# Kernel optimization log

Hardware: AMD Instinct MI355X
Metric: run time of the kernel (lower is better)

## Reference

```python
import jax, jax.numpy as jnp
import numpy as np

B, S, D, H = 4, 2048, 2048, 16
DH = D // H  # 128
BASE = 10000.0


def _rope_tables(seq_len, d_head, dtype):
    # inv_freq over even indices of half-dim, freqs duplicated (cat(freqs, freqs))
    inv_freq = 1.0 / (BASE ** (jnp.arange(0, d_head, 2, dtype=jnp.float32) / d_head))
    t = jnp.arange(seq_len, dtype=jnp.float32)
    freqs = jnp.einsum('i,j->ij', t, inv_freq)          # [S, d_head/2]
    emb = jnp.concatenate([freqs, freqs], axis=-1)       # [S, d_head]
    return jnp.cos(emb).astype(dtype), jnp.sin(emb).astype(dtype)


def _rotate_half(x):
    x1, x2 = jnp.split(x, 2, axis=-1)
    return jnp.concatenate([-x2, x1], axis=-1)


def setup_inputs() -> dict:
    key = jax.random.key(0)
    k1, k2, k3 = jax.random.split(key, 3)
    x = jax.random.normal(k1, (B, S, D), dtype=jnp.float32)
    Wqkv = jax.random.normal(k2, (3 * D, D), dtype=jnp.float32) * (D ** -0.5)
    Wo = jax.random.normal(k3, (D, D), dtype=jnp.float32) * (D ** -0.5)
    return {"x": x, "Wqkv": Wqkv, "Wo": Wo}


def reference(x, Wqkv, Wo) -> jnp.ndarray:
    b, s, d = x.shape
    # fused QKV projection: Linear(d, 3d, bias=False) -> x @ Wqkv.T
    qkv = jnp.einsum('bsd,ed->bse', x, Wqkv)                      # [B,S,3D]
    qkv = qkv.reshape(b, s, 3, H, DH)                              # (n n_head d_head)
    q = jnp.transpose(qkv[:, :, 0], (0, 2, 1, 3))                  # [B,H,S,DH]
    k = jnp.transpose(qkv[:, :, 1], (0, 2, 1, 3))
    v = jnp.transpose(qkv[:, :, 2], (0, 2, 1, 3))
    # rotary position embedding
    cos, sin = _rope_tables(s, DH, x.dtype)                        # [S,DH]
    cos = cos[None, None, :, :]
    sin = sin[None, None, :, :]
    q = q * cos + _rotate_half(q) * sin
    k = k * cos + _rotate_half(k) * sin
    # eval-path manual causal attention
    scale = 1.0 / jnp.sqrt(jnp.asarray(DH, dtype=x.dtype))
    scores = jnp.einsum('bhqd,bhkd->bhqk', q, k) * scale           # [B,H,S,S]
    causal = jnp.tril(jnp.ones((s, s), dtype=bool))
    scores = jnp.where(causal[None, None, :, :], scores, -jnp.inf)
    pattern = jax.nn.softmax(scores, axis=-1)
    z = jnp.einsum('bhqk,bhkd->bhqd', pattern, v)                  # [B,H,S,DH]
    z = jnp.transpose(z, (0, 2, 1, 3)).reshape(b, s, d)            # [B,S,D]
    return jnp.einsum('bsd,ed->bse', z, Wo)
```

## Files before the change

### kernel.cpp

```cpp
#include <hip/hip_runtime.h>
#include <hip/hip_bf16.h>
#include <stdint.h>

#define B_ 4
#define S_ 2048
#define D_ 2048
#define H_ 16
#define DH_ 128

typedef short bf8_t __attribute__((ext_vector_type(8)));
typedef float f4_t  __attribute__((ext_vector_type(4)));

__device__ __forceinline__ unsigned short f2bf(float f) {
  __hip_bfloat16 h = __float2bfloat16(f);
  return *reinterpret_cast<const unsigned short*>(&h);
}
__device__ __forceinline__ float bf2f(unsigned short u) {
  return __uint_as_float(((unsigned int)u) << 16);
}

__device__ __forceinline__ void gload_lds16(const void* g, void* lds) {
  __builtin_amdgcn_global_load_lds(
      (const __attribute__((address_space(1))) unsigned int*)(uintptr_t)g,
      (__attribute__((address_space(3))) unsigned int*)(unsigned int)(uintptr_t)lds,
      16, 0, 0);
}

__global__ __launch_bounds__(256) void conv_bf16(const float* __restrict__ in,
                                                 unsigned short* __restrict__ out,
                                                 int n4) {
  int i = blockIdx.x * 256 + threadIdx.x;
  if (i >= n4) return;
  float4 v = ((const float4*)in)[i];
  ushort4 u;
  u.x = f2bf(v.x); u.y = f2bf(v.y); u.z = f2bf(v.z); u.w = f2bf(v.w);
  ((ushort4*)out)[i] = u;
}

template <int EPI>
__global__ __launch_bounds__(512, 2) void gemm256(
    const unsigned short* __restrict__ A, const unsigned short* __restrict__ Bt,
    float* __restrict__ Cf, unsigned short* __restrict__ Cb,
    int M, int N, int K) {
  __shared__ unsigned short AB[4][2][8192];
  const int tid  = threadIdx.x;
  const int lane = tid & 63;
  const int wv   = tid >> 6;
  const int wr   = wv >> 2;
  const int wc   = wv & 3;
  const int rsel = lane & 15;
  const int g    = lane >> 4;
  const int qr0  = g * 4;

  int id  = blockIdx.y * gridDim.x + blockIdx.x;
  int cpx = (gridDim.x * gridDim.y) >> 3;
  int swz = (id & 7) * cpx + (id >> 3);
  const int bm = (swz / gridDim.x) * 256;
  const int bn = (swz % gridDim.x) * 256;

  const int NS = K >> 5;

  const int ob0 = tid * 16, ob1 = ob0 + 8192;
  const int row0 = ob0 >> 6, row1 = ob1 >> 6;
  const int g0 = ((ob0 >> 4) & 3) ^ ((row0 >> 1) & 3);
  const int g1 = ((ob1 >> 4) & 3) ^ ((row1 >> 1) & 3);
  const unsigned short* Ag0 = A + (size_t)(bm + row0) * K + g0 * 8;
  const unsigned short* Ag1 = A + (size_t)(bm + row1) * K + g1 * 8;
  const unsigned short* Bg0 = Bt + (size_t)(bn + row0) * K + g0 * 8;
  const unsigned short* Bg1 = Bt + (size_t)(bn + row1) * K + g1 * 8;

  f4_t acc[8][4];
#pragma unroll
  for (int i = 0; i < 8; ++i)
#pragma unroll
    for (int j = 0; j < 4; ++j) acc[i][j] = (f4_t){0.f, 0.f, 0.f, 0.f};

  int aoff[8], boff[4];
#pragma unroll
  for (int i = 0; i < 8; ++i) {
    int arow = wr * 128 + i * 16 + rsel;
    aoff[i] = arow * 64 + ((g * 16) ^ ((arow & 6) << 3));
  }
#pragma unroll
  for (int j = 0; j < 4; ++j) {
    int brow = wc * 64 + j * 16 + rsel;
    boff[j] = brow * 64 + ((g * 16) ^ ((brow & 6) << 3));
  }

#define STAGE(sl)                                                        \
  {                                                                      \
    int slot_ = (sl) & 3;                                                \
    int ks_   = (sl) << 5;                                               \
    gload_lds16(Ag0 + ks_, (char*)&AB[slot_][0][0] + ob0);               \
    gload_lds16(Ag1 + ks_, (char*)&AB[slot_][0][0] + ob1);               \
    gload_lds16(Bg0 + ks_, (char*)&AB[slot_][1][0] + ob0);               \
    gload_lds16(Bg1 + ks_, (char*)&AB[slot_][1][0] + ob1);               \
  }

  STAGE(0); STAGE(1); STAGE(2);

  for (int s = 0; s < NS; ++s) {
    if (s < NS - 2)       asm volatile("s_waitcnt vmcnt(8)" ::: "memory");
    else if (s == NS - 2) asm volatile("s_waitcnt vmcnt(4)" ::: "memory");
    else                  asm volatile("s_waitcnt vmcnt(0)" ::: "memory");
    __builtin_amdgcn_s_barrier();
    asm volatile("" ::: "memory");

    const char* As_ = (const char*)&AB[s & 3][0][0];
    const char* Bs_ = (const char*)&AB[s & 3][1][0];
    bf8_t af[8], bfr[4];
#pragma unroll
    for (int i = 0; i < 8; ++i) af[i] = *(const bf8_t*)(As_ + aoff[i]);
#pragma unroll
    for (int j = 0; j < 4; ++j) bfr[j] = *(const bf8_t*)(Bs_ + boff[j]);

    if (s + 3 < NS) STAGE(s + 3);

    __builtin_amdgcn_s_setprio(1);
#pragma unroll
    for (int i = 0; i < 8; ++i)
#pragma unroll
      for (int j = 0; j < 4; ++j)
        acc[i][j] = __builtin_amdgcn_mfma_f32_16x16x32_bf16(af[i], bfr[j], acc[i][j], 0, 0, 0);
    __builtin_amdgcn_s_setprio(0);
  }
#undef STAGE

#pragma unroll
  for (int i = 0; i < 8; ++i) {
#pragma unroll
    for (int j = 0; j < 4; ++j) {
#pragma unroll
      for (int r = 0; r < 4; ++r) {
        int row = bm + wr * 128 + i * 16 + qr0 + r;
        int col = bn + wc * 64 + j * 16 + rsel;
        float v = acc[i][j][r];
        if (EPI == 0) {
          Cf[(size_t)row * N + col] = v;
        } else {
          int c = col >> 11, h = (col >> 7) & (H_ - 1), dh = col & (DH_ - 1);
          int b = row >> 11, s = row & (S_ - 1);
          size_t dst = ((((size_t)c * B_ + b) * H_ + h) * S_ + s) * DH_ + dh;
          Cb[dst] = f2bf(v);
        }
      }
    }
  }
}

__global__ void rope_tab(float* __restrict__ tc, float* __restrict__ ts) {
  int s = blockIdx.x;
  int i = threadIdx.x;
  float inv = powf(10000.0f, -(float)i / 64.0f);
  float f   = (float)s * inv;
  tc[s * 64 + i] = cosf(f);
  ts[s * 64 + i] = sinf(f);
}

__global__ __launch_bounds__(256) void rope_apply(
    unsigned short* __restrict__ Q, unsigned short* __restrict__ Kk,
    const float* __restrict__ tc, const float* __restrict__ ts) {
  int idx  = blockIdx.x * 256 + threadIdx.x;
  int i    = idx & 63;
  int s    = (idx >> 6) & (S_ - 1);
  int bh   = (idx >> 17) & 63;
  int tsel = idx >> 23;
  unsigned short* T = tsel ? Kk : Q;
  size_t base = ((size_t)bh * S_ + s) * DH_;
  float x1 = bf2f(T[base + i]);
  float x2 = bf2f(T[base + i + 64]);
  float c  = tc[s * 64 + i], sn = ts[s * 64 + i];
  T[base + i]      = f2bf(x1 * c - x2 * sn);
  T[base + i + 64] = f2bf(x2 * c + x1 * sn);
}

__global__ __launch_bounds__(512) void attn_fwd(
    const unsigned short* __restrict__ Q, const unsigned short* __restrict__ Kk,
    const unsigned short* __restrict__ V, unsigned short* __restrict__ Z) {
  __shared__ unsigned short Ks[3][64 * 128];
  __shared__ unsigned short Vt[2][128 * 64];
  __shared__ unsigned short Pw[8][16 * 64];
  const int tid  = threadIdx.x;
  const int lane = tid & 63;
  const int wv   = tid >> 6;

  int id = blockIdx.y * gridDim.x + blockIdx.x;
  int sw = (id & 7) * ((gridDim.x * gridDim.y) >> 3) + (id >> 3);
  const int bh = sw >> 4;
  const int q0 = (15 - (sw & 15)) * 128;

  const size_t base = (size_t)bh * S_ * DH_;
  const int rsel = lane & 15;
  const int g    = lane >> 4;
  const int kof  = g * 8;
  const int qr0  = g * 4;
  const int qlo  = q0 + wv * 16;
  const int qhi  = qlo + 15;
  const int qrow = qlo + rsel;
  const float sl2 = 0.08838834764831845f * 1.4426950408889634f;

  bf8_t aq[4];
#pragma unroll
  for (int kc = 0; kc < 4; ++kc) {
    aq[kc] = *(const bf8_t*)&Q[base + (size_t)qrow * DH_ + kc * 32 + kof];
#pragma unroll
    for (int e = 0; e < 8; ++e)
      aq[kc][e] = (short)f2bf(bf2f((unsigned short)aq[kc][e]) * sl2);
  }

  bf8_t vones;
#pragma unroll
  for (int e = 0; e < 8; ++e) vones[e] = (short)0x3F80;

  f4_t o[9];
#pragma unroll
  for (int nf = 0; nf < 9; ++nf) o[nf] = (f4_t){0.f, 0.f, 0.f, 0.f};
  float mrow[4] = {-3e30f, -3e30f, -3e30f, -3e30f};
  const int nt = q0 / 64 + 2;

  const int kvp = tid & 31;
  const int vc0 = (tid >> 5) * 8;

#define KSTAGE(tt)                                                            \
  {                                                                           \
    const unsigned short* gK_ = Kk + base + (size_t)(tt) * 64 * DH_;          \
    int slot_ = (tt) % 3;                                                     \
    _Pragma("unroll")                                                         \
    for (int c = 0; c < 2; ++c) {                                             \
      int ob = (c * 512 + tid) * 16;                                          \
      int row = ob >> 8;                                                      \
      int scol = (ob & 255) ^ ((row & 7) << 4);                               \
      gload_lds16(gK_ + (size_t)row * DH_ + (scol >> 1),                      \
                  (char*)&Ks[slot_][0] + ob);                                 \
    }                                                                         \
  }
#define VTWRITE(buf_)                                                         \
  {                                                                           \
    unsigned int* Vt32 = (unsigned int*)&Vt[buf_][0];                         \
    _Pragma("unroll")                                                         \
    for (int e = 0; e < 8; ++e) {                                             \
      unsigned int val = (unsigned short)vlo[e] |                             \
                         ((unsigned int)(unsigned short)vhi[e] << 16);        \
      Vt32[(vc0 + e) * 32 + (kvp ^ (e << 2))] = val;                          \
    }                                                                         \
  }

  bf8_t vlo, vhi;
  vlo = *(const bf8_t*)&V[base + (size_t)(2 * kvp) * DH_ + vc0];
  vhi = *(const bf8_t*)&V[base + (size_t)(2 * kvp + 1) * DH_ + vc0];
  KSTAGE(0);
  KSTAGE(1);
  VTWRITE(0);

  for (int t = 0; t < nt; ++t) {
    const int curV = t & 1;
    const int curK = t % 3;
    const bool pfV = (t + 1 < nt);
    const bool pfK = (t + 2 < nt);

    if (pfV) asm volatile("s_waitcnt vmcnt(2)" ::: "memory");
    else     asm volatile("s_waitcnt vmcnt(0)" ::: "memory");
    asm volatile("s_waitcnt lgkmcnt(0)" ::: "memory");
    __builtin_amdgcn_s_barrier();
    asm volatile("" ::: "memory");

    if (pfV) {
      const unsigned short* gV = V + base + (size_t)(t + 1) * 64 * DH_;
      vlo = *(const bf8_t*)&gV[(size_t)(2 * kvp) * DH_ + vc0];
      vhi = *(const bf8_t*)&gV[(size_t)(2 * kvp + 1) * DH_ + vc0];
    }
    if (pfK) KSTAGE(t + 2);

    const int kv0 = t * 64;
    const bool active = (kv0 <= qhi);
    const bool domask = active && (kv0 + 63 > qlo);

    if (active) {
      f4_t sacc[4];
#pragma unroll
      for (int cf = 0; cf < 4; ++cf) sacc[cf] = (f4_t){0.f, 0.f, 0.f, 0.f};
      __builtin_amdgcn_s_setprio(1);
#pragma unroll
      for (int cf = 0; cf < 4; ++cf)
#pragma unroll
        for (int kc = 0; kc < 4; ++kc) {
          int krow = cf * 16 + rsel;
          bf8_t bk = *(const bf8_t*)&Ks[curK][krow * 128 + ((kc * 32 + kof) ^ ((krow & 7) << 3))];
          sacc[cf] = __builtin_amdgcn_mfma_f32_16x16x32_bf16(aq[kc], bk, sacc[cf], 0, 0, 0);
        }
      __builtin_amdgcn_s_setprio(0);

      if (domask) {
#pragma unroll
        for (int cf = 0; cf < 4; ++cf) {
          int kvabs = kv0 + cf * 16 + rsel;
#pragma unroll
          for (int r = 0; r < 4; ++r) {
            int qabs = qlo + qr0 + r;
            if (kvabs > qabs) sacc[cf][r] = -3e30f;
          }
        }
      }

      float tmr[4];
#pragma unroll
      for (int r = 0; r < 4; ++r)
        tmr[r] = fmaxf(fmaxf(sacc[0][r], sacc[1][r]), fmaxf(sacc[2][r], sacc[3][r]));
      bool needr = (tmr[0] > mrow[0] + 11.f) || (tmr[1] > mrow[1] + 11.f) ||
                   (tmr[2] > mrow[2] + 11.f) || (tmr[3] > mrow[3] + 11.f);
      if (__any(needr)) {
#pragma unroll
        for (int r = 0; r < 4; ++r) {
          float m = tmr[r];
#pragma unroll
          for (int d = 1; d < 16; d <<= 1) m = fmaxf(m, __shfl_xor(m, d, 16));
          float nm = fmaxf(mrow[r], m);
          float sc = exp2f(mrow[r] - nm);
          mrow[r] = nm;
#pragma unroll
          for (int nf = 0; nf < 9; ++nf) o[nf][r] *= sc;
        }
      }
#pragma unroll
      for (int cf = 0; cf < 4; ++cf)
#pragma unroll
        for (int r = 0; r < 4; ++r)
          sacc[cf][r] = exp2f(sacc[cf][r] - mrow[r]);

      unsigned short* P = &Pw[wv][0];
#pragma unroll
      for (int cf = 0; cf < 4; ++cf)
#pragma unroll
        for (int r = 0; r < 4; ++r) {
          int prow = qr0 + r;
          P[prow * 64 + ((cf * 16 + rsel) ^ ((prow >> 1) << 3))] = f2bf(sacc[cf][r]);
        }
    }

    if (pfV) VTWRITE(curV ^ 1);

    if (active) {
      unsigned short* P = &Pw[wv][0];
      __builtin_amdgcn_s_setprio(1);
#pragma unroll
      for (int kc2 = 0; kc2 < 2; ++kc2) {
        bf8_t pa = *(const bf8_t*)&P[rsel * 64 + ((kc2 * 32 + kof) ^ ((rsel >> 1) << 3))];
#pragma unroll
        for (int nf = 0; nf < 8; ++nf) {
          int vrow = nf * 16 + rsel;
          bf8_t bv = *(const bf8_t*)&Vt[curV][vrow * 64 + ((kc2 * 32 + kof) ^ ((vrow & 7) << 3))];
          o[nf] = __builtin_amdgcn_mfma_f32_16x16x32_bf16(pa, bv, o[nf], 0, 0, 0);
        }
        o[8] = __builtin_amdgcn_mfma_f32_16x16x32_bf16(pa, vones, o[8], 0, 0, 0);
      }
      __builtin_amdgcn_s_setprio(0);
    }
  }
#undef KSTAGE
#undef VTWRITE

  const int b = bh >> 4, h = bh & 15;
#pragma unroll
  for (int r = 0; r < 4; ++r) {
    float inv = 1.0f / o[8][r];
    int s = qlo + qr0 + r;
    size_t rowo = ((size_t)b * S_ + s) * D_ + h * DH_;
#pragma unroll
    for (int nf = 0; nf < 8; ++nf)
      Z[rowo + nf * 16 + rsel] = f2bf(o[nf][r] * inv);
  }
}

extern "C" void kernel_launch(void* const* d_in, const int* in_sizes, int n_in,
                              void* d_out, int out_size, void* d_ws, size_t ws_size,
                              hipStream_t stream) {
  const float* x    = (const float*)d_in[0];
  const float* Wqkv = (const float*)d_in[1];
  const float* Wo   = (const float*)d_in[2];
  float* out = (float*)d_out;

  const size_t QKV_ELEMS = (size_t)B_ * H_ * S_ * DH_;
  char* w = (char*)d_ws;
  unsigned short* xb = (unsigned short*)w;
  unsigned short* z  = xb;
  w += (size_t)8192 * 2048 * 2;
  unsigned short* wqkvb = (unsigned short*)w; w += (size_t)6144 * 2048 * 2;
  unsigned short* wob   = (unsigned short*)w; w += (size_t)2048 * 2048 * 2;
  unsigned short* qq = (unsigned short*)w;    w += QKV_ELEMS * 2;
  unsigned short* kk = (unsigned short*)w;    w += QKV_ELEMS * 2;
  unsigned short* vv = (unsigned short*)w;    w += QKV_ELEMS * 2;
  float* tabc = (float*)w; w += (size_t)S_ * 64 * 4;
  float* tabs = (float*)w; w += (size_t)S_ * 64 * 4;
  if ((size_t)(w - (char*)d_ws) > ws_size) return;

  conv_bf16<<<16384, 256, 0, stream>>>(x, xb, 8192 * 2048 / 4);
  conv_bf16<<<12288, 256, 0, stream>>>(Wqkv, wqkvb, 6144 * 2048 / 4);
  conv_bf16<<<4096, 256, 0, stream>>>(Wo, wob, 2048 * 2048 / 4);
  gemm256<1><<<dim3(24, 32), 512, 0, stream>>>(xb, wqkvb, nullptr, qq, 8192, 6144, 2048);
  rope_tab<<<2048, 64, 0, stream>>>(tabc, tabs);
  rope_apply<<<65536, 256, 0, stream>>>(qq, kk, tabc, tabs);
  attn_fwd<<<dim3(S_ / 128, B_ * H_), 512, 0, stream>>>(qq, kk, vv, z);
  gemm256<0><<<dim3(8, 32), 512, 0, stream>>>(z, wob, out, nullptr, 8192, 2048, 2048);
}
```

Baseline: 495.7 us.

## Process 32 query rows per wave to double K/V tile reuse in attention

Result: faster. 431.1 us (-13.0%).

```diff
diff --git a/kernel.cpp b/kernel.cpp
--- a/kernel.cpp
+++ b/kernel.cpp
@@ -179,44 +179,51 @@
     const unsigned short* __restrict__ V, unsigned short* __restrict__ Z) {
   __shared__ unsigned short Ks[3][64 * 128];
   __shared__ unsigned short Vt[2][128 * 64];
-  __shared__ unsigned short Pw[8][16 * 64];
+  __shared__ unsigned short Pw[8][32 * 64];
   const int tid  = threadIdx.x;
   const int lane = tid & 63;
   const int wv   = tid >> 6;
 
-  int id = blockIdx.y * gridDim.x + blockIdx.x;
-  int sw = (id & 7) * ((gridDim.x * gridDim.y) >> 3) + (id >> 3);
-  const int bh = sw >> 4;
-  const int q0 = (15 - (sw & 15)) * 128;
+  int id  = blockIdx.y * gridDim.x + blockIdx.x;
+  int x   = id & 7;
+  int idx = id >> 3;
+  const int bh = x * 8 + (idx & 7);
+  const int q0 = (7 - (idx >> 3)) * 256;
 
   const size_t base = (size_t)bh * S_ * DH_;
   const int rsel = lane & 15;
   const int g    = lane >> 4;
   const int kof  = g * 8;
   const int qr0  = g * 4;
-  const int qlo  = q0 + wv * 16;
-  const int qhi  = qlo + 15;
-  const int qrow = qlo + rsel;
+  const int qlo  = q0 + wv * 32;
+  const int qhi  = qlo + 31;
   const float sl2 = 0.08838834764831845f * 1.4426950408889634f;
 
-  bf8_t aq[4];
-#pragma unroll
-  for (int kc = 0; kc < 4; ++kc) {
-    aq[kc] = *(const bf8_t*)&Q[base + (size_t)qrow * DH_ + kc * 32 + kof];
-#pragma unroll
-    for (int e = 0; e < 8; ++e)
-      aq[kc][e] = (short)f2bf(bf2f((unsigned short)aq[kc][e]) * sl2);
+  bf8_t aq[2][4];
+#pragma unroll
+  for (int rg = 0; rg < 2; ++rg) {
+    const int qrow = qlo + rg * 16 + rsel;
+#pragma unroll
+    for (int kc = 0; kc < 4; ++kc) {
+      aq[rg][kc] = *(const bf8_t*)&Q[base + (size_t)qrow * DH_ + kc * 32 + kof];
+#pragma unroll
+      for (int e = 0; e < 8; ++e)
+        aq[rg][kc][e] = (short)f2bf(bf2f((unsigned short)aq[rg][kc][e]) * sl2);
+    }
   }
 
   bf8_t vones;
 #pragma unroll
   for (int e = 0; e < 8; ++e) vones[e] = (short)0x3F80;
 
-  f4_t o[9];
-#pragma unroll
-  for (int nf = 0; nf < 9; ++nf) o[nf] = (f4_t){0.f, 0.f, 0.f, 0.f};
-  float mrow[4] = {-3e30f, -3e30f, -3e30f, -3e30f};
-  const int nt = q0 / 64 + 2;
+  f4_t o[2][9];
+#pragma unroll
+  for (int rg = 0; rg < 2; ++rg)
+#pragma unroll
+    for (int nf = 0; nf < 9; ++nf) o[rg][nf] = (f4_t){0.f, 0.f, 0.f, 0.f};
+  float mrow[2][4] = {{-3e30f, -3e30f, -3e30f, -3e30f},
+                      {-3e30f, -3e30f, -3e30f, -3e30f}};
+  const int nt = q0 / 64 + 4;
 
   const int kvp = tid & 31;
   const int vc0 = (tid >> 5) * 8;
@@ -276,9 +283,11 @@
     const bool domask = active && (kv0 + 63 > qlo);
 
     if (active) {
-      f4_t sacc[4];
-#pragma unroll
-      for (int cf = 0; cf < 4; ++cf) sacc[cf] = (f4_t){0.f, 0.f, 0.f, 0.f};
+      f4_t sacc[2][4];
+#pragma unroll
+      for (int rg = 0; rg < 2; ++rg)
+#pragma unroll
+        for (int cf = 0; cf < 4; ++cf) sacc[rg][cf] = (f4_t){0.f, 0.f, 0.f, 0.f};
       __builtin_amdgcn_s_setprio(1);
 #pragma unroll
       for (int cf = 0; cf < 4; ++cf)
@@ -286,55 +295,68 @@
         for (int kc = 0; kc < 4; ++kc) {
           int krow = cf * 16 + rsel;
           bf8_t bk = *(const bf8_t*)&Ks[curK][krow * 128 + ((kc * 32 + kof) ^ ((krow & 7) << 3))];
-          sacc[cf] = __builtin_amdgcn_mfma_f32_16x16x32_bf16(aq[kc], bk, sacc[cf], 0, 0, 0);
+          sacc[0][cf] = __builtin_amdgcn_mfma_f32_16x16x32_bf16(aq[0][kc], bk, sacc[0][cf], 0, 0, 0);
+          sacc[1][cf] = __builtin_amdgcn_mfma_f32_16x16x32_bf16(aq[1][kc], bk, sacc[1][cf], 0, 0, 0);
         }
       __builtin_amdgcn_s_setprio(0);
 
       if (domask) {
 #pragma unroll
-        for (int cf = 0; cf < 4; ++cf) {
-          int kvabs = kv0 + cf * 16 + rsel;
+        for (int rg = 0; rg < 2; ++rg)
+#pragma unroll
+          for (int cf = 0; cf < 4; ++cf) {
+            int kvabs = kv0 + cf * 16 + rsel;
+#pragma unroll
+            for (int r = 0; r < 4; ++r) {
+              int qabs = qlo + rg * 16 + qr0 + r;
+              if (kvabs > qabs) sacc[rg][cf][r] = -3e30f;
+            }
+          }
+      }
+
+      float tmr[2][4];
+      bool needr = false;
+#pragma unroll
+      for (int rg = 0; rg < 2; ++rg)
+#pragma unroll
+        for (int r = 0; r < 4; ++r) {
+          tmr[rg][r] = fmaxf(fmaxf(sacc[rg][0][r], sacc[rg][1][r]),
+                             fmaxf(sacc[rg][2][r], sacc[rg][3][r]));
+          needr = needr || (tmr[rg][r] > mrow[rg][r] + 11.f);
+        }
+      if (__any(needr)) {
+#pragma unroll
+        for (int rg = 0; rg < 2; ++rg)
 #pragma unroll
           for (int r = 0; r < 4; ++r) {
-            int qabs = qlo + qr0 + r;
-            if (kvabs > qabs) sacc[cf][r] = -3e30f;
+            float m = tmr[rg][r];
+#pragma unroll
+            for (int d = 1; d < 16; d <<= 1) m = fmaxf(m, __shfl_xor(m, d, 16));
+            float nm = fmaxf(mrow[rg][r], m);
+            float sc = exp2f(mrow[rg][r] - nm);
+            mrow[rg][r] = nm;
+#pragma unroll
+            for (int nf = 0; nf < 9; ++nf) o[rg][nf][r] *= sc;
           }
-        }
       }
-
-      float tmr[4];
-#pragma unroll
-      for (int r = 0; r < 4; ++r)
-        tmr[r] = fmaxf(fmaxf(sacc[0][r], sacc[1][r]), fmaxf(sacc[2][r], sacc[3][r]));
-      bool needr = (tmr[0] > mrow[0] + 11.f) || (tmr[1] > mrow[1] + 11.f) ||
-                   (tmr[2] > mrow[2] + 11.f) || (tmr[3] > mrow[3] + 11.f);
-      if (__any(needr)) {
-#pragma unroll
-        for (int r = 0; r < 4; ++r) {
-          float m = tmr[r];
-#pragma unroll
-          for (int d = 1; d < 16; d <<= 1) m = fmaxf(m, __shfl_xor(m, d, 16));
-          float nm = fmaxf(mrow[r], m);
-          float sc = exp2f(mrow[r] - nm);
-          mrow[r] = nm;
-#pragma unroll
-          for (int nf = 0; nf < 9; ++nf) o[nf][r] *= sc;
-        }
-      }
-#pragma unroll
-      for (int cf = 0; cf < 4; ++cf)
-#pragma unroll
-        for (int r = 0; r < 4; ++r)
-          sacc[cf][r] = exp2f(sacc[cf][r] - mrow[r]);
+#pragma unroll
+      for (int rg = 0; rg < 2; ++rg)
+#pragma unroll
+        for (int cf = 0; cf < 4; ++cf)
+#pragma unroll
+          for (int r = 0; r < 4; ++r)
+            sacc[rg][cf][r] = exp2f(sacc[rg][cf][r] - mrow[rg][r]);
 
       unsigned short* P = &Pw[wv][0];
 #pragma unroll
-      for (int cf = 0; cf < 4; ++cf)
-#pragma unroll
-        for (int r = 0; r < 4; ++r) {
-          int prow = qr0 + r;
-          P[prow * 64 + ((cf * 16 + rsel) ^ ((prow >> 1) << 3))] = f2bf(sacc[cf][r]);
-        }
+      for (int rg = 0; rg < 2; ++rg)
+#pragma unroll
+        for (int cf = 0; cf < 4; ++cf)
+#pragma unroll
+          for (int r = 0; r < 4; ++r) {
+            int prow = rg * 16 + qr0 + r;
+            P[prow * 64 + ((cf * 16 + rsel) ^ (((prow >> 1) & 7) << 3))] = f2bf(sacc[rg][cf][r]);
+          }
     }
 
     if (pfV) VTWRITE(curV ^ 1);
@@ -344,14 +366,22 @@
       __builtin_amdgcn_s_setprio(1);
 #pragma unroll
       for (int kc2 = 0; kc2 < 2; ++kc2) {
-        bf8_t pa = *(const bf8_t*)&P[rsel * 64 + ((kc2 * 32 + kof) ^ ((rsel >> 1) << 3))];
+        bf8_t pa0, pa1;
+        {
+          int pr0 = rsel;
+          int pr1 = 16 + rsel;
+          pa0 = *(const bf8_t*)&P[pr0 * 64 + ((kc2 * 32 + kof) ^ (((pr0 >> 1) & 7) << 3))];
+          pa1 = *(const bf8_t*)&P[pr1 * 64 + ((kc2 * 32 + kof) ^ (((pr1 >> 1) & 7) << 3))];
+        }
 #pragma unroll
         for (int nf = 0; nf < 8; ++nf) {
           int vrow = nf * 16 + rsel;
           bf8_t bv = *(const bf8_t*)&Vt[curV][vrow * 64 + ((kc2 * 32 + kof) ^ ((vrow & 7) << 3))];
-          o[nf] = __builtin_amdgcn_mfma_f32_16x16x32_bf16(pa, bv, o[nf], 0, 0, 0);
+          o[0][nf] = __builtin_amdgcn_mfma_f32_16x16x32_bf16(pa0, bv, o[0][nf], 0, 0, 0);
+          o[1][nf] = __builtin_amdgcn_mfma_f32_16x16x32_bf16(pa1, bv, o[1][nf], 0, 0, 0);
         }
-        o[8] = __builtin_amdgcn_mfma_f32_16x16x32_bf16(pa, vones, o[8], 0, 0, 0);
+        o[0][8] = __builtin_amdgcn_mfma_f32_16x16x32_bf16(pa0, vones, o[0][8], 0, 0, 0);
+        o[1][8] = __builtin_amdgcn_mfma_f32_16x16x32_bf16(pa1, vones, o[1][8], 0, 0, 0);
       }
       __builtin_amdgcn_s_setprio(0);
     }
@@ -361,14 +391,16 @@
 
   const int b = bh >> 4, h = bh & 15;
 #pragma unroll
-  for (int r = 0; r < 4; ++r) {
-    float inv = 1.0f / o[8][r];
-    int s = qlo + qr0 + r;
-    size_t rowo = ((size_t)b * S_ + s) * D_ + h * DH_;
-#pragma unroll
-    for (int nf = 0; nf < 8; ++nf)
-      Z[rowo + nf * 16 + rsel] = f2bf(o[nf][r] * inv);
-  }
+  for (int rg = 0; rg < 2; ++rg)
+#pragma unroll
+    for (int r = 0; r < 4; ++r) {
+      float inv = 1.0f / o[rg][8][r];
+      int s = qlo + rg * 16 + qr0 + r;
+      size_t rowo = ((size_t)b * S_ + s) * D_ + h * DH_;
+#pragma unroll
+      for (int nf = 0; nf < 8; ++nf)
+        Z[rowo + nf * 16 + rsel] = f2bf(o[rg][nf][r] * inv);
+    }
 }
 
 extern "C" void kernel_launch(void* const* d_in, const int* in_sizes, int n_in,
@@ -399,6 +431,6 @@
   gemm256<1><<<dim3(24, 32), 512, 0, stream>>>(xb, wqkvb, nullptr, qq, 8192, 6144, 2048);
   rope_tab<<<2048, 64, 0, stream>>>(tabc, tabs);
   rope_apply<<<65536, 256, 0, stream>>>(qq, kk, tabc, tabs);
-  attn_fwd<<<dim3(S_ / 128, B_ * H_), 512, 0, stream>>>(qq, kk, vv, z);
+  attn_fwd<<<dim3(S_ / 256, B_ * H_), 512, 0, stream>>>(qq, kk, vv, z);
   gemm256<0><<<dim3(8, 32), 512, 0, stream>>>(z, wob, out, nullptr, 8192, 2048, 2048);
 }
```
